# Optimization experiments

Measured on AMD Instinct MI355X. Metric: run time of the kernel, lower is better.

## Reference

```python
import jax, jax.numpy as jnp
import numpy as np

N_STARS = 2048   # n_stars
BATCH = 256      # query positions per call
PF = 28          # poly_features = (d_max+1)(d_max+2)/2, d_max=6
NGE = 512        # n_graph_elems
GF = 32          # graph_features
OPD = 256        # opd_dim


def setup_inputs() -> dict:
    key = jax.random.key(0)
    ks = jax.random.split(key, 8)
    # observed star positions in the FoV (x_lims/y_lims = [0,1000])
    obs_pos = jax.random.uniform(ks[0], (N_STARS, 2), jnp.float32, 0.0, 1000.0)
    # query positions are exact rows of obs_pos (required by the exact-match index search)
    idx = jax.random.randint(ks[1], (BATCH,), 0, N_STARS)
    positions = obs_pos[idx]
    poly_dic = jax.random.normal(ks[2], (N_STARS, PF), jnp.float32)
    graph_dic = jax.random.normal(ks[3], (N_STARS, NGE), jnp.float32)
    # alpha matrices: identity(-padded) init as in init_vars, plus small noise
    alpha_poly = jnp.eye(PF, dtype=jnp.float32) + 0.01 * jax.random.normal(ks[4], (PF, PF), jnp.float32)
    alpha_graph = (jnp.eye(NGE, GF, dtype=jnp.float32)
                   + 0.01 * jax.random.normal(ks[5], (NGE, GF), jnp.float32))
    # S features: random uniform in [-1e-3, 1e-3] as in init_vars
    S_poly = jax.random.uniform(ks[6], (PF, OPD, OPD), jnp.float32, -0.001, 0.001)
    S_graph = jax.random.uniform(ks[7], (GF, OPD, OPD), jnp.float32, -0.001, 0.001)
    return {
        'positions': positions, 'obs_pos': obs_pos,
        'poly_dic': poly_dic, 'graph_dic': graph_dic,
        'alpha_poly': alpha_poly, 'alpha_graph': alpha_graph,
        'S_poly': S_poly, 'S_graph': S_graph,
    }


def _calc_indices(positions, obs_pos):
    # Faithful to tf.where(tf.equal(obs_pos, pos))[0, 0]: first True entry (row-major)
    # of the elementwise equality over (n_stars, 2); its row index is taken.
    eq = positions[:, None, :] == obs_pos[None, :, :]          # (B, N, 2) bool
    flat_first = jnp.argmax(eq.reshape(eq.shape[0], -1), axis=1)  # first True, flat index
    return flat_first // 2                                      # row index in obs_pos


def reference(positions, obs_pos, poly_dic, graph_dic, alpha_poly, alpha_graph, S_poly, S_graph):
    indices = _calc_indices(positions, obs_pos)                 # (B,) int
    # polynomial part: gather -> matmul -> tensordot with OPD modes
    batch_poly = jnp.take(poly_dic, indices, axis=0)            # (B, PF)
    interm_poly = batch_poly @ alpha_poly                       # (B, PF)
    contrib_poly = jnp.einsum('bp,pij->bij', interm_poly, S_poly)  # (B, OPD, OPD)
    # graph part
    batch_graph = jnp.take(graph_dic, indices, axis=0)          # (B, NGE)
    interm_graph = batch_graph @ alpha_graph                    # (B, GF)
    contrib_graph = jnp.einsum('bg,gij->bij', interm_graph, S_graph)
    return contrib_poly + contrib_graph
```

## Files before the change

### kernel.cpp

```cpp
#include <hip/hip_runtime.h>

#define NSTARS 2048
#define BATCH  256
#define PF     28
#define NGE    512
#define GF     32
#define OPD2   65536
#define KTOT   (PF + GF)
#define NTILE  4096

#define WA_OFF 61440
#define WA_HALF 32768
#define SB_OFF (WA_OFF + 2 * WA_HALF)
#define SB_BYTES ((size_t)NTILE * 2 * 64 * 16)
#define WS_NEED (SB_OFF + SB_BYTES)

typedef float f32x4 __attribute__((ext_vector_type(4)));
typedef short bf16x8 __attribute__((ext_vector_type(8)));
typedef unsigned int u32;

__global__ __launch_bounds__(256) void prep_kernel(
    const float* __restrict__ positions,  const float* __restrict__ obs_pos,
    const float* __restrict__ poly_dic,   const float* __restrict__ graph_dic,
    const float* __restrict__ alpha_poly, const float* __restrict__ alpha_graph,
    float* __restrict__ Wt)
{
    const int b = blockIdx.x;
    const int t = threadIdx.x;

    const float p0 = positions[2 * b];
    const float p1 = positions[2 * b + 1];

    int cand = 0x7fffffff;
    #pragma unroll
    for (int i = 0; i < NSTARS / 256; ++i) {
        const int n = t + i * 256;
        const float o0 = obs_pos[2 * n];
        const float o1 = obs_pos[2 * n + 1];
        if (o0 == p0 || o1 == p1) cand = min(cand, n);
    }
    __shared__ int smin[256];
    smin[t] = cand;
    __syncthreads();
    for (int s = 128; s > 0; s >>= 1) {
        if (t < s) smin[t] = min(smin[t], smin[t + s]);
        __syncthreads();
    }
    int idx = smin[0];
    if (idx == 0x7fffffff) idx = 0;

    if (t < PF) {
        float acc = 0.f;
        #pragma unroll
        for (int p = 0; p < PF; ++p)
            acc += poly_dic[idx * PF + p] * alpha_poly[p * PF + t];
        Wt[t * BATCH + b] = acc;
    }

    __shared__ float psum[8][GF];
    {
        const int g = t & 31;
        const int r = t >> 5;
        float acc = 0.f;
        const int e0 = r * (NGE / 8);
        for (int e = e0; e < e0 + NGE / 8; ++e)
            acc += graph_dic[idx * NGE + e] * alpha_graph[e * GF + g];
        psum[r][g] = acc;
    }
    __syncthreads();
    if (t < GF) {
        float acc = 0.f;
        #pragma unroll
        for (int r = 0; r < 8; ++r) acc += psum[r][t];
        Wt[(PF + t) * BATCH + b] = acc;
    }
}

__device__ __forceinline__ u32 bf16_rne(u32 x) {
    return (x + 0x7FFFu + ((x >> 16) & 1u)) >> 16;
}
__device__ __forceinline__ float bf16_to_f32(u32 h) {
    return __uint_as_float(h << 16);
}

__global__ __launch_bounds__(256) void prep2_kernel(
    const float* __restrict__ Wt, u32* __restrict__ Wa_hi, u32* __restrict__ Wa_lo)
{
    const int f     = blockIdx.x * 256 + threadIdx.x;
    const int lane  = f & 63;
    const int kf    = (f >> 6) & 1;
    const int mtile = f >> 7;
    const int m     = mtile * 16 + (lane & 15);
    const int kbase = kf * 32 + (lane >> 4) * 8;
    u32 hi_pk[4], lo_pk[4];
    #pragma unroll
    for (int p = 0; p < 4; ++p) {
        u32 h[2], l[2];
        #pragma unroll
        for (int q = 0; q < 2; ++q) {
            const int k = kbase + 2 * p + q;
            float w = (k < KTOT) ? Wt[k * BATCH + m] : 0.f;
            const u32 hb = bf16_rne(__float_as_uint(w));
            const float resid = w - bf16_to_f32(hb);
            h[q] = hb;
            l[q] = bf16_rne(__float_as_uint(resid));
        }
        hi_pk[p] = h[0] | (h[1] << 16);
        lo_pk[p] = l[0] | (l[1] << 16);
    }
    *reinterpret_cast<f32x4*>(Wa_hi + f * 4) = *reinterpret_cast<f32x4*>(hi_pk);
    *reinterpret_cast<f32x4*>(Wa_lo + f * 4) = *reinterpret_cast<f32x4*>(lo_pk);
}

__global__ __launch_bounds__(256) void conv_kernel(
    const float* __restrict__ S_poly, const float* __restrict__ S_graph,
    u32* __restrict__ Sb)
{
    const int f    = blockIdx.x * 256 + threadIdx.x;
    const int lane = f & 63;
    const int kf   = (f >> 6) & 1;
    const int tile = f >> 7;
    const int ij   = tile * 16 + (lane & 15);
    const int kbase = kf * 32 + (lane >> 4) * 8;
    u32 pk[4];
    #pragma unroll
    for (int p = 0; p < 4; ++p) {
        u32 b16[2];
        #pragma unroll
        for (int q = 0; q < 2; ++q) {
            const int k = kbase + 2 * p + q;
            u32 v = 0u;
            if (k < KTOT) {
                const float s = (k < PF) ? S_poly[(size_t)k * OPD2 + ij]
                                         : S_graph[(size_t)(k - PF) * OPD2 + ij];
                v = bf16_rne(__float_as_uint(s));
            }
            b16[q] = v;
        }
        pk[p] = b16[0] | (b16[1] << 16);
    }
    *reinterpret_cast<f32x4*>(Sb + (size_t)f * 4) = *reinterpret_cast<f32x4*>(pk);
}

__global__ __launch_bounds__(256) void mfma_kernel(
    const u32* __restrict__ Sb, const u32* __restrict__ Wa_hi,
    const u32* __restrict__ Wa_lo, float* __restrict__ out)
{
    const int t    = threadIdx.x;
    const int id   = blockIdx.x;
    const int xcd  = id & 7;
    const int slot = id >> 3;
    const int xb   = xcd * 32 + (slot & 31);
    const int yb   = slot >> 5;
    const int w    = t >> 6;
    const int lane = t & 63;
    const int b0   = yb * 64;
    const int Tb   = xb * 16 + w * 4;

    bf16x8 Ah[4][2], Al[4][2];
    #pragma unroll
    for (int mt = 0; mt < 4; ++mt)
        #pragma unroll
        for (int kf = 0; kf < 2; ++kf) {
            const int fi = (((yb * 4 + mt) * 2 + kf) * 64 + lane) * 4;
            Ah[mt][kf] = *reinterpret_cast<const bf16x8*>(Wa_hi + fi);
            Al[mt][kf] = *reinterpret_cast<const bf16x8*>(Wa_lo + fi);
        }

    const int row = (lane >> 4) * 4;
    const int col = lane & 15;

    #pragma unroll
    for (int tt = 0; tt < 4; ++tt) {
        const int T = Tb + tt;
        const bf16x8 B0 = *reinterpret_cast<const bf16x8*>(
            Sb + ((size_t)(T * 2 + 0) * 64 + lane) * 4);
        const bf16x8 B1 = *reinterpret_cast<const bf16x8*>(
            Sb + ((size_t)(T * 2 + 1) * 64 + lane) * 4);
        #pragma unroll
        for (int mt = 0; mt < 4; ++mt) {
            f32x4 acc = (f32x4)(0.f);
            acc = __builtin_amdgcn_mfma_f32_16x16x32_bf16(Al[mt][0], B0, acc, 0, 0, 0);
            acc = __builtin_amdgcn_mfma_f32_16x16x32_bf16(Al[mt][1], B1, acc, 0, 0, 0);
            acc = __builtin_amdgcn_mfma_f32_16x16x32_bf16(Ah[mt][0], B0, acc, 0, 0, 0);
            acc = __builtin_amdgcn_mfma_f32_16x16x32_bf16(Ah[mt][1], B1, acc, 0, 0, 0);
            float* op = out + (size_t)(b0 + mt * 16 + row) * OPD2 + T * 16 + col;
            #pragma unroll
            for (int j = 0; j < 4; ++j)
                __builtin_nontemporal_store(acc[j], op + (size_t)j * OPD2);
        }
    }
}

__global__ __launch_bounds__(256) void fb_kernel(
    const float* __restrict__ S_poly, const float* __restrict__ S_graph,
    const float* __restrict__ Wt, float* __restrict__ out)
{
    const int t  = threadIdx.x;
    const int ij = blockIdx.x * 1024 + t * 4;
    const int b0 = blockIdx.y * 16;
    f32x4 acc[16];
    #pragma unroll
    for (int b = 0; b < 16; ++b) acc[b] = (f32x4)(0.f);
    const float* __restrict__ wp = Wt + b0;
    #pragma unroll 2
    for (int k = 0; k < PF; ++k) {
        const f32x4 s = *reinterpret_cast<const f32x4*>(S_poly + (size_t)k * OPD2 + ij);
        #pragma unroll
        for (int b = 0; b < 16; ++b) acc[b] += wp[k * BATCH + b] * s;
    }
    #pragma unroll 2
    for (int k = 0; k < GF; ++k) {
        const f32x4 s = *reinterpret_cast<const f32x4*>(S_graph + (size_t)k * OPD2 + ij);
        #pragma unroll
        for (int b = 0; b < 16; ++b) acc[b] += wp[(PF + k) * BATCH + b] * s;
    }
    #pragma unroll
    for (int b = 0; b < 16; ++b)
        *reinterpret_cast<f32x4*>(out + (size_t)(b0 + b) * OPD2 + ij) = acc[b];
}

extern "C" void kernel_launch(void* const* d_in, const int* in_sizes, int n_in,
                              void* d_out, int out_size, void* d_ws, size_t ws_size,
                              hipStream_t stream) {
    const float* positions   = (const float*)d_in[0];
    const float* obs_pos     = (const float*)d_in[1];
    const float* poly_dic    = (const float*)d_in[2];
    const float* graph_dic   = (const float*)d_in[3];
    const float* alpha_poly  = (const float*)d_in[4];
    const float* alpha_graph = (const float*)d_in[5];
    const float* S_poly      = (const float*)d_in[6];
    const float* S_graph     = (const float*)d_in[7];
    float* out = (float*)d_out;

    float* Wt = (float*)d_ws;

    prep_kernel<<<BATCH, 256, 0, stream>>>(positions, obs_pos, poly_dic,
                                           graph_dic, alpha_poly, alpha_graph,
                                           Wt);

    if (ws_size >= WS_NEED) {
        u32* Wa_hi = (u32*)((char*)d_ws + WA_OFF);
        u32* Wa_lo = (u32*)((char*)d_ws + WA_OFF + WA_HALF);
        u32* Sb    = (u32*)((char*)d_ws + SB_OFF);
        prep2_kernel<<<8, 256, 0, stream>>>(Wt, Wa_hi, Wa_lo);
        conv_kernel<<<2048, 256, 0, stream>>>(S_poly, S_graph, Sb);
        mfma_kernel<<<1024, 256, 0, stream>>>(Sb, Wa_hi, Wa_lo, out);
    } else {
        dim3 grid(OPD2 / 1024, BATCH / 16);
        fb_kernel<<<grid, 256, 0, stream>>>(S_poly, S_graph, Wt, out);
    }
}
```

Baseline: 123.3 us.

## Fuse S bf16 conversion into MFMA kernel via shared-memory fragments

Removes the separate conv_kernel that converted S_poly/S_graph to packed bf16 MFMA fragments in global workspace. Each MFMA block now loads its own 256-column slice of S, converts it to bf16 and stages the fragments in LDS before the matrix multiply. This drops one kernel launch and the global write and re-read of the converted S buffer. The cost is that S is re-read and re-converted once per batch block (4x redundancy), plus an LDS barrier and more shared-memory use.

```diff
diff --git a/kernel.cpp b/kernel.cpp
--- a/kernel.cpp
+++ b/kernel.cpp
@@ -7,13 +7,10 @@
 #define GF     32
 #define OPD2   65536
 #define KTOT   (PF + GF)
-#define NTILE  4096
 
 #define WA_OFF 61440
 #define WA_HALF 32768
-#define SB_OFF (WA_OFF + 2 * WA_HALF)
-#define SB_BYTES ((size_t)NTILE * 2 * 64 * 16)
-#define WS_NEED (SB_OFF + SB_BYTES)
+#define WS_NEED (WA_OFF + 2 * WA_HALF)
 
 typedef float f32x4 __attribute__((ext_vector_type(4)));
 typedef short bf16x8 __attribute__((ext_vector_type(8)));
@@ -112,40 +109,13 @@
     *reinterpret_cast<f32x4*>(Wa_lo + f * 4) = *reinterpret_cast<f32x4*>(lo_pk);
 }
 
-__global__ __launch_bounds__(256) void conv_kernel(
+__global__ __launch_bounds__(256) void mfma_kernel(
     const float* __restrict__ S_poly, const float* __restrict__ S_graph,
-    u32* __restrict__ Sb)
-{
-    const int f    = blockIdx.x * 256 + threadIdx.x;
-    const int lane = f & 63;
-    const int kf   = (f >> 6) & 1;
-    const int tile = f >> 7;
-    const int ij   = tile * 16 + (lane & 15);
-    const int kbase = kf * 32 + (lane >> 4) * 8;
-    u32 pk[4];
-    #pragma unroll
-    for (int p = 0; p < 4; ++p) {
-        u32 b16[2];
-        #pragma unroll
-        for (int q = 0; q < 2; ++q) {
-            const int k = kbase + 2 * p + q;
-            u32 v = 0u;
-            if (k < KTOT) {
-                const float s = (k < PF) ? S_poly[(size_t)k * OPD2 + ij]
-                                         : S_graph[(size_t)(k - PF) * OPD2 + ij];
-                v = bf16_rne(__float_as_uint(s));
-            }
-            b16[q] = v;
-        }
-        pk[p] = b16[0] | (b16[1] << 16);
-    }
-    *reinterpret_cast<f32x4*>(Sb + (size_t)f * 4) = *reinterpret_cast<f32x4*>(pk);
-}
-
-__global__ __launch_bounds__(256) void mfma_kernel(
-    const u32* __restrict__ Sb, const u32* __restrict__ Wa_hi,
-    const u32* __restrict__ Wa_lo, float* __restrict__ out)
-{
+    const u32* __restrict__ Wa_hi, const u32* __restrict__ Wa_lo,
+    float* __restrict__ out)
+{
+    __shared__ u32 sfrag[32 * 256];
+
     const int t    = threadIdx.x;
     const int id   = blockIdx.x;
     const int xcd  = id & 7;
@@ -155,7 +125,33 @@
     const int w    = t >> 6;
     const int lane = t & 63;
     const int b0   = yb * 64;
-    const int Tb   = xb * 16 + w * 4;
+    const int ij0  = xb * 256;
+
+    #pragma unroll
+    for (int i = 0; i < 8; ++i) {
+        const int f    = w * 8 + i;
+        const int tile = f >> 1;
+        const int kf   = f & 1;
+        const int ij   = ij0 + tile * 16 + (lane & 15);
+        const int kb   = kf * 32 + (lane >> 4) * 8;
+        u32 pk[4];
+        #pragma unroll
+        for (int p = 0; p < 4; ++p) {
+            u32 lo = 0u, hi = 0u;
+            const int k0 = kb + 2 * p, k1 = k0 + 1;
+            if (k0 < KTOT)
+                lo = bf16_rne(__float_as_uint(
+                    k0 < PF ? S_poly[(size_t)k0 * OPD2 + ij]
+                            : S_graph[(size_t)(k0 - PF) * OPD2 + ij]));
+            if (k1 < KTOT)
+                hi = bf16_rne(__float_as_uint(
+                    k1 < PF ? S_poly[(size_t)k1 * OPD2 + ij]
+                            : S_graph[(size_t)(k1 - PF) * OPD2 + ij]));
+            pk[p] = lo | (hi << 16);
+        }
+        *reinterpret_cast<f32x4*>(&sfrag[f * 256 + lane * 4]) =
+            *reinterpret_cast<f32x4*>(pk);
+    }
 
     bf16x8 Ah[4][2], Al[4][2];
     #pragma unroll
@@ -167,16 +163,19 @@
             Al[mt][kf] = *reinterpret_cast<const bf16x8*>(Wa_lo + fi);
         }
 
+    __syncthreads();
+
     const int row = (lane >> 4) * 4;
     const int col = lane & 15;
 
     #pragma unroll
     for (int tt = 0; tt < 4; ++tt) {
-        const int T = Tb + tt;
+        const int lt = w * 4 + tt;
+        const int T  = xb * 16 + lt;
         const bf16x8 B0 = *reinterpret_cast<const bf16x8*>(
-            Sb + ((size_t)(T * 2 + 0) * 64 + lane) * 4);
+            &sfrag[(lt * 2 + 0) * 256 + lane * 4]);
         const bf16x8 B1 = *reinterpret_cast<const bf16x8*>(
-            Sb + ((size_t)(T * 2 + 1) * 64 + lane) * 4);
+            &sfrag[(lt * 2 + 1) * 256 + lane * 4]);
         #pragma unroll
         for (int mt = 0; mt < 4; ++mt) {
             f32x4 acc = (f32x4)(0.f);
@@ -242,10 +241,8 @@
     if (ws_size >= WS_NEED) {
         u32* Wa_hi = (u32*)((char*)d_ws + WA_OFF);
         u32* Wa_lo = (u32*)((char*)d_ws + WA_OFF + WA_HALF);
-        u32* Sb    = (u32*)((char*)d_ws + SB_OFF);
         prep2_kernel<<<8, 256, 0, stream>>>(Wt, Wa_hi, Wa_lo);
-        conv_kernel<<<2048, 256, 0, stream>>>(S_poly, S_graph, Sb);
-        mfma_kernel<<<1024, 256, 0, stream>>>(Sb, Wa_hi, Wa_lo, out);
+        mfma_kernel<<<1024, 256, 0, stream>>>(S_poly, S_graph, Wa_hi, Wa_lo, out);
     } else {
         dim3 grid(OPD2 / 1024, BATCH / 16);
         fb_kernel<<<grid, 256, 0, stream>>>(S_poly, S_graph, Wt, out);
```

Result: no change. 123.7 us (+0.3%).
